# Kernel optimization log

Measured on AMD Instinct MI355X. Metric: run time of the kernel, lower is better.

Reference implementation:

```python
import jax, jax.numpy as jnp
import numpy as np

D = 1024
H = 16
HD = D // H
B = 2
S = 2048


def setup_inputs() -> dict:
    key = jax.random.key(0)
    ks = jax.random.split(key, 9)
    sc = 1.0 / np.sqrt(D)
    return {
        "x": jax.random.normal(ks[0], (B, S, D), dtype=jnp.float32),
        "attention_mask": jnp.ones((B, S), dtype=jnp.int32),
        "Wq": jax.random.normal(ks[1], (D, D), dtype=jnp.float32) * sc,
        "bq": jax.random.normal(ks[2], (D,), dtype=jnp.float32) * 0.02,
        "Wk": jax.random.normal(ks[3], (D, D), dtype=jnp.float32) * sc,
        "bk": jax.random.normal(ks[4], (D,), dtype=jnp.float32) * 0.02,
        "Wv": jax.random.normal(ks[5], (D, D), dtype=jnp.float32) * sc,
        "bv": jax.random.normal(ks[6], (D,), dtype=jnp.float32) * 0.02,
        "Wo": jax.random.normal(ks[7], (D, D), dtype=jnp.float32) * sc,
        "bo": jax.random.normal(ks[8], (D,), dtype=jnp.float32) * 0.02,
    }


def reference(x, attention_mask, Wq, bq, Wk, bk, Wv, bv, Wo, bo):
    Bb, Ss, d = x.shape
    # projections (torch Linear: x @ W.T + b; here W stored as [in,out])
    q = (x @ Wq + bq).reshape(Bb, Ss, H, HD).transpose(0, 2, 1, 3)  # [B,H,S,hd]
    k = (x @ Wk + bk).reshape(Bb, Ss, H, HD).transpose(0, 2, 1, 3)
    v = (x @ Wv + bv).reshape(Bb, Ss, H, HD).transpose(0, 2, 1, 3)
    dots = jnp.einsum("bhqd,bhkd->bhqk", q, k) / np.sqrt(HD)  # [B,H,S,S]
    causal = jnp.triu(jnp.ones((Ss, Ss), dtype=bool), k=1)  # True above diagonal
    dots = jnp.where(causal[None, None], -jnp.inf, dots)
    pad = (attention_mask == 0)[:, None, None, :]  # [B,1,1,S]
    dots = jnp.where(pad, -jnp.inf, dots)
    scores = jax.nn.softmax(dots, axis=-1)
    o = jnp.einsum("bhqk,bhkd->bhqd", scores, v)  # [B,H,S,hd]
    o = o.transpose(0, 2, 1, 3).reshape(Bb, Ss, d)
    return o @ Wo + bo
```

## Files before the change

kernel.cpp:

```cpp
#include <hip/hip_runtime.h>

#define D_  1024
#define H_  16
#define HD_ 64
#define B_  2
#define S_  2048
#define M_  (B_*S_)

typedef _Float16 f16;
typedef _Float16 f16x8 __attribute__((ext_vector_type(8)));
typedef _Float16 f16x4 __attribute__((ext_vector_type(4)));
typedef _Float16 f16x2 __attribute__((ext_vector_type(2)));
typedef __fp16   h16x2 __attribute__((ext_vector_type(2)));
typedef float    f32x4 __attribute__((ext_vector_type(4)));

#define GLOAD_LDS16(g, l) \
  __builtin_amdgcn_global_load_lds((__attribute__((address_space(1))) const void*)(g), \
                                   (__attribute__((address_space(3))) void*)(l), 16, 0, 0)

__global__ void k_cvt_x(const float* __restrict__ x, f16* __restrict__ xb) {
  int i = blockIdx.x * blockDim.x + threadIdx.x;
  float4 v = ((const float4*)x)[i];
  f16x4 o = { (f16)v.x, (f16)v.y, (f16)v.z, (f16)v.w };
  ((f16x4*)xb)[i] = o;
}

__global__ void k_twt4(const float* __restrict__ Wq, const float* __restrict__ Wk,
                       const float* __restrict__ Wv, const float* __restrict__ Wo,
                       f16* __restrict__ WT) {
  __shared__ float t[32][33];
  int z = blockIdx.z;
  const float* W = (z == 0) ? Wq : (z == 1) ? Wk : (z == 2) ? Wv : Wo;
  f16* out = WT + (size_t)z * D_ * D_;
  int n0 = blockIdx.x * 32, k0 = blockIdx.y * 32;
  int tx = threadIdx.x, ty = threadIdx.y;
  #pragma unroll
  for (int i = 0; i < 4; i++)
    t[ty + i*8][tx] = W[(size_t)(k0 + ty + i*8) * D_ + n0 + tx];
  __syncthreads();
  #pragma unroll
  for (int i = 0; i < 4; i++)
    out[(size_t)(n0 + ty + i*8) * D_ + k0 + tx] = (f16)t[tx][ty + i*8];
}

template<int MODE>
__device__ __forceinline__ void gemm_body(const f16* __restrict__ A,
                                          const f16* __restrict__ Bt,
                                          const float* __restrict__ bias,
                                          void* __restrict__ Cout) {
  __shared__ __align__(16) f16 lA[2][128 * 32];
  __shared__ __align__(16) f16 lB[2][128 * 32];
  const int tid = threadIdx.x;
  const int wv = tid >> 6, lane = tid & 63;
  const int m0 = blockIdx.y * 128, n0 = blockIdx.x * 128;
  const int fr = lane & 15, fg = lane >> 4;
  const int wm = wv >> 1, wn = wv & 1;
  const int srow = (lane >> 2), skk = (lane & 3) * 8;
  f32x4 acc[4][4] = {};

#define G_STAGE(k0_, c_) do { \
    _Pragma("unroll") \
    for (int it_ = 0; it_ < 2; ++it_) { \
      int ch_ = wv + it_ * 4; \
      int row_ = ch_ * 16 + srow; \
      GLOAD_LDS16(A  + (size_t)(m0 + row_) * D_ + (k0_) + skk, &lA[c_][ch_ * 512]); \
      GLOAD_LDS16(Bt + (size_t)(n0 + row_) * D_ + (k0_) + skk, &lB[c_][ch_ * 512]); \
    } \
  } while (0)

  G_STAGE(0, 0);
  __syncthreads();

  int c = 0;
  for (int k0 = 0; k0 < D_; k0 += 32) {
    if (k0 + 32 < D_) G_STAGE(k0 + 32, c ^ 1);
    f16x8 a[4], b[4];
    #pragma unroll
    for (int i = 0; i < 4; i++) a[i] = *(const f16x8*)&lA[c][(wm*64 + i*16 + fr) * 32 + fg * 8];
    #pragma unroll
    for (int j = 0; j < 4; j++) b[j] = *(const f16x8*)&lB[c][(wn*64 + j*16 + fr) * 32 + fg * 8];
    #pragma unroll
    for (int i = 0; i < 4; i++)
      #pragma unroll
      for (int j = 0; j < 4; j++)
        acc[i][j] = __builtin_amdgcn_mfma_f32_16x16x32_f16(a[i], b[j], acc[i][j], 0, 0, 0);
    __syncthreads();
    c ^= 1;
  }
#undef G_STAGE

  #pragma unroll
  for (int i = 0; i < 4; i++) {
    #pragma unroll
    for (int j = 0; j < 4; j++) {
      int grow0 = m0 + wm*64 + i*16 + fg*4;
      int gcol  = n0 + wn*64 + j*16 + fr;
      float bb = bias[gcol & (D_ - 1)];
      #pragma unroll
      for (int r = 0; r < 4; r++) {
        float val = acc[i][j][r] + bb;
        int grow = grow0 + r;
        if (MODE == 0) {
          int z = gcol >> 10, gl = gcol & (D_ - 1);
          int b = grow >> 11, s = grow & (S_ - 1);
          int h = gl >> 6,  hd = gl & (HD_ - 1);
          ((f16*)Cout)[(size_t)z * (M_ * D_) +
                       ((size_t)(b * H_ + h) * S_ + s) * HD_ + hd] = (f16)val;
        } else {
          ((float*)Cout)[(size_t)grow * D_ + gcol] = val;
        }
      }
    }
  }
}

__global__ __launch_bounds__(256) void k_gemm_qkv(const f16* __restrict__ A,
                                                  const f16* __restrict__ WT0,
                                                  const float* __restrict__ bq,
                                                  const float* __restrict__ bk,
                                                  const float* __restrict__ bv,
                                                  f16* __restrict__ qkv) {
  const int n0 = blockIdx.x * 128;
  const float* bias = (n0 < 1024) ? bq : (n0 < 2048) ? bk : bv;
  gemm_body<0>(A, WT0, bias, qkv);
}

__global__ __launch_bounds__(256) void k_gemm_out(const f16* __restrict__ A,
                                                  const f16* __restrict__ Bt,
                                                  const float* __restrict__ bias,
                                                  float* __restrict__ Cout) {
  gemm_body<1>(A, Bt, bias, Cout);
}

#define POFF 8.65617025f

__global__ __launch_bounds__(256) void k_attn(const f16* __restrict__ Qh,
                                              const f16* __restrict__ Kh,
                                              const f16* __restrict__ Vh,
                                              const int* __restrict__ am,
                                              f16* __restrict__ OpA, f16* __restrict__ OpB,
                                              float* __restrict__ lpA, float* __restrict__ lpB) {
  __shared__ __align__(16) f16 kt[2][64 * 64];
  __shared__ __align__(16) f16 vt[2][64 * 64];
  __shared__ __align__(16) f16 pl[4][32 * 64];

  const int tid = threadIdx.x;
  const int wv = tid >> 6, lane = tid & 63;
  const int fr = lane & 15, fg = lane >> 4;

  const int d = blockIdx.x;
  const int bh = d & 31;
  const int m  = (d >> 5) & 7;
  const int typeB = d >> 8;
  const int b = bh >> 4, h = bh & 15;
  (void)h;

  f16*   Op = typeB ? OpB : OpA;
  float* lp = typeB ? lpB : lpA;

  const f16* Qb = Qh + (size_t)bh * S_ * HD_;
  const f16* Kb = Kh + (size_t)bh * S_ * HD_;
  const f16* Vb = Vh + (size_t)bh * S_ * HD_;
  const int* amb = am + b * S_;
  f16* plw = pl[wv];

  volatile int* flag = (volatile int*)&pl[0][0];
  if (tid == 0) *flag = 1;
  __syncthreads();
  {
    int mv = 1;
    #pragma unroll
    for (int i = 0; i < 8; ++i) mv &= amb[tid * 8 + i];
    if (!mv) *flag = 0;
  }
  __syncthreads();
  const bool allv = (*flag != 0);

  const f16 qs = (f16)0.18033688f;
  const int ksrc = 8 * ((lane & 7) ^ (lane >> 3));
  const int swz = (fr & 7) << 3;
  const int vkk = (tid >> 3) * 2, vd0 = (tid & 7) * 8;
  const int vswz2 = (tid & 3) << 4;
  const f32x4 cinit = { -POFF, -POFF, -POFF, -POFF };
  const f16 one_ = (f16)1.0f;
  const f16x8 onesf = { one_, one_, one_, one_, one_, one_, one_, one_ };

#define STAGE_K(t_, c_) do { \
    const f16* kp_ = Kb + (size_t)((t_) * 64) * HD_; \
    GLOAD_LDS16(kp_ + (size_t)((wv*2+0)*8 + (lane >> 3)) * HD_ + ksrc, &kt[c_][(wv*2+0)*512]); \
    GLOAD_LDS16(kp_ + (size_t)((wv*2+1)*8 + (lane >> 3)) * HD_ + ksrc, &kt[c_][(wv*2+1)*512]); \
  } while (0)

#define LOAD_V(t_) do { \
    const f16* vp_ = Vb + (size_t)((t_) * 64 + vkk) * HD_ + vd0; \
    vA = *(const f16x8*)vp_; vBr = *(const f16x8*)(vp_ + HD_); \
  } while (0)

#define WRITE_V(c_) do { \
    _Pragma("unroll") \
    for (int j_ = 0; j_ < 8; ++j_) { \
      f16x2 pr_ = { vA[j_], vBr[j_] }; \
      *(f16x2*)&vt[c_][(vd0 + j_) * 64 + ((vkk ^ (j_ << 3)) ^ vswz2)] = pr_; \
    } \
  } while (0)

  f16x8 vA, vBr;

  auto run_half = [&](int qt, int t0, int t1) {
    const int q0w = qt * 128 + wv * 32;

    f16x8 qf[2][2];
    #pragma unroll
    for (int rt = 0; rt < 2; ++rt) {
      f16x8 r0 = *(const f16x8*)&Qb[(size_t)(q0w + rt*16 + fr) * HD_ + fg*8];
      f16x8 r1 = *(const f16x8*)&Qb[(size_t)(q0w + rt*16 + fr) * HD_ + 32 + fg*8];
      qf[rt][0] = r0 * qs; qf[rt][1] = r1 * qs;
    }

    f32x4 accO[2][4] = {};
    f32x4 accL[2] = {};

    STAGE_K(t0, 0);
    LOAD_V(t0);
    WRITE_V(0);
    __syncthreads();

    int c = 0;
    for (int t = t0; t < t1; ++t) {
      const int kb = t * 64;
      const bool pre = (t + 1 < t1);
      if (pre) { STAGE_K(t + 1, c ^ 1); LOAD_V(t + 1); }

      const int dq = q0w - kb;
      if (dq + 31 >= 0) {
        int tm1 = (dq + 31) >> 4; if (tm1 > 3) tm1 = 3;
        int tm0 = (dq + 15) >> 4; if (tm0 > 3) tm0 = 3;
        const bool fullb = (dq >= 63);

        f32x4 s[2][4];
        #pragma unroll
        for (int rt = 0; rt < 2; ++rt)
          #pragma unroll
          for (int tt = 0; tt < 4; ++tt) s[rt][tt] = cinit;

        __builtin_amdgcn_s_setprio(1);
        #pragma unroll
        for (int tt = 0; tt < 4; ++tt) {
          if (tt <= tm1) {
            const int kr = (tt*16 + fr) * 64;
            f16x8 kf0 = *(const f16x8*)&kt[c][kr + ((     fg*8) ^ swz)];
            f16x8 kf1 = *(const f16x8*)&kt[c][kr + ((32 + fg*8) ^ swz)];
            s[1][tt] = __builtin_amdgcn_mfma_f32_16x16x32_f16(kf0, qf[1][0], s[1][tt], 0, 0, 0);
            s[1][tt] = __builtin_amdgcn_mfma_f32_16x16x32_f16(kf1, qf[1][1], s[1][tt], 0, 0, 0);
            if (tt <= tm0) {
              s[0][tt] = __builtin_amdgcn_mfma_f32_16x16x32_f16(kf0, qf[0][0], s[0][tt], 0, 0, 0);
              s[0][tt] = __builtin_amdgcn_mfma_f32_16x16x32_f16(kf1, qf[0][1], s[0][tt], 0, 0, 0);
            }
          }
        }
        __builtin_amdgcn_s_setprio(0);

        #pragma unroll
        for (int rt = 0; rt < 2; ++rt) {
          const int tmr = rt ? tm1 : tm0;
          if (tmr < 0) continue;
          const int thr = dq + rt*16 + fr;
          #pragma unroll
          for (int tt = 0; tt < 4; ++tt) {
            union { f16x4 v; h16x2 h[2]; } pk;
            pk.v = (f16x4){};
            if (tt <= tmr) {
              float p[4];
              if (allv) {
                #pragma unroll
                for (int r = 0; r < 4; ++r) {
                  float sv = s[rt][tt][r];
                  if (!fullb) sv = (tt*16 + fg*4 + r <= thr) ? sv : -1e30f;
                  p[r] = exp2f(sv);
                }
              } else {
                int4 a4 = *(const int4*)&amb[kb + tt*16 + fg*4];
                #pragma unroll
                for (int r = 0; r < 4; ++r) {
                  float sv = s[rt][tt][r];
                  if (!fullb) sv = (tt*16 + fg*4 + r <= thr) ? sv : -1e30f;
                  float pv = exp2f(sv);
                  int mr_ = (r == 0) ? a4.x : (r == 1) ? a4.y : (r == 2) ? a4.z : a4.w;
                  p[r] = mr_ ? pv : 0.0f;
                }
              }
              pk.h[0] = __builtin_amdgcn_cvt_pkrtz(p[0], p[1]);
              pk.h[1] = __builtin_amdgcn_cvt_pkrtz(p[2], p[3]);
            }
            *(f16x4*)&plw[(rt*16 + fr) * 64 + ((tt*16 + fg*4) ^ swz)] = pk.v;
          }
        }

        __builtin_amdgcn_s_setprio(1);
        #pragma unroll
        for (int ks = 0; ks < 2; ++ks) {
          if (ks <= (tm1 >> 1)) {
            f16x8 vf[4];
            #pragma unroll
            for (int nt = 0; nt < 4; ++nt)
              vf[nt] = *(const f16x8*)&vt[c][(nt*16 + fr) * 64 +
                           ((ks*32 + fg*8) ^ swz ^ (((2*nt + (fr >> 3)) & 3) << 4))];
            #pragma unroll
            for (int rt = 0; rt < 2; ++rt) {
              const int tmr = rt ? tm1 : tm0;
              if (tmr >= 0 && ks <= (tmr >> 1)) {
                f16x8 pa = *(const f16x8*)&plw[(rt*16 + fr) * 64 + ((ks*32 + fg*8) ^ swz)];
                #pragma unroll
                for (int nt = 0; nt < 4; ++nt)
                  accO[rt][nt] = __builtin_amdgcn_mfma_f32_16x16x32_f16(pa, vf[nt], accO[rt][nt], 0, 0, 0);
                accL[rt] = __builtin_amdgcn_mfma_f32_16x16x32_f16(pa, onesf, accL[rt], 0, 0, 0);
              }
            }
          }
        }
        __builtin_amdgcn_s_setprio(0);
      }

      if (pre) WRITE_V(c ^ 1);
      __syncthreads();
      c ^= 1;
    }

    #pragma unroll
    for (int rt = 0; rt < 2; ++rt) {
      if (fr == 0) {
        #pragma unroll
        for (int r = 0; r < 4; ++r)
          lp[(size_t)bh * S_ + q0w + rt*16 + fg*4 + r] = accL[rt][r];
      }
      f16* Oprow = Op + (size_t)bh * (S_ * HD_);
      #pragma unroll
      for (int nt = 0; nt < 4; ++nt) {
        int col = nt*16 + fr;
        #pragma unroll
        for (int r = 0; r < 4; ++r) {
          int row = q0w + rt*16 + fg*4 + r;
          Oprow[(size_t)row * HD_ + col] = (f16)accO[rt][nt][r];
        }
      }
    }
  };

  const int qtA = m, qtB = 15 - m;
  if (!typeB) {
    run_half(qtA, 0, qtA + 1);
    run_half(qtB, 0, qtB + 1);
  } else {
    run_half(qtA, qtA + 1, 2 * (qtA + 1));
    run_half(qtB, qtB + 1, 2 * (qtB + 1));
  }

#undef STAGE_K
#undef LOAD_V
#undef WRITE_V
}

__global__ __launch_bounds__(256) void k_comb(const f16* __restrict__ OA,
                                              const f16* __restrict__ OB,
                                              const float* __restrict__ lA,
                                              const float* __restrict__ lB,
                                              f16* __restrict__ Obf) {
  int gid = blockIdx.x * 256 + threadIdx.x;
  int seg = gid & 7, rowg = gid >> 3;
  int bh = rowg >> 11, row = rowg & 2047;
  f16x8 a  = ((const f16x8*)OA)[gid];
  f16x8 b2 = ((const f16x8*)OB)[gid];
  float inv = __builtin_amdgcn_rcpf(lA[rowg] + lB[rowg]);
  f16x8 o;
  #pragma unroll
  for (int j = 0; j < 8; ++j) o[j] = (f16)(((float)a[j] + (float)b2[j]) * inv);
  int bb = bh >> 4, hh = bh & 15;
  *(f16x8*)&Obf[((size_t)(bb * S_ + row)) * D_ + hh * 64 + seg * 8] = o;
}

extern "C" void kernel_launch(void* const* d_in, const int* in_sizes, int n_in,
                              void* d_out, int out_size, void* d_ws, size_t ws_size,
                              hipStream_t stream) {
  const float* x  = (const float*)d_in[0];
  const int*   am = (const int*)d_in[1];
  const float* Wq = (const float*)d_in[2];
  const float* bq = (const float*)d_in[3];
  const float* Wk = (const float*)d_in[4];
  const float* bk = (const float*)d_in[5];
  const float* Wv = (const float*)d_in[6];
  const float* bv = (const float*)d_in[7];
  const float* Wo = (const float*)d_in[8];
  const float* bo = (const float*)d_in[9];

  char* ws = (char*)d_ws;
  f16*   xb  = (f16*)(ws);
  f16*   wt  = (f16*)(ws + (8u  << 20));
  f16*   qkv = (f16*)(ws + (16u << 20));
  f16*   OpA = (f16*)(ws + (40u << 20));
  f16*   OpB = xb;
  float* lpA = (float*)(ws + (8u << 20));
  float* lpB = (float*)(ws + (8u << 20) + (256u << 10));
  f16*   Obf = qkv;

  k_cvt_x<<<4096, 256, 0, stream>>>(x, xb);

  dim3 tb(32, 8), tg4(32, 32, 4);
  k_twt4<<<tg4, tb, 0, stream>>>(Wq, Wk, Wv, Wo, wt);

  k_gemm_qkv<<<dim3(24, 32), 256, 0, stream>>>(xb, wt, bq, bk, bv, qkv);

  k_attn<<<dim3(512), 256, 0, stream>>>(qkv,
                                        qkv + (size_t)M_ * D_,
                                        qkv + 2 * (size_t)M_ * D_,
                                        am, OpA, OpB, lpA, lpB);

  k_comb<<<dim3(2048), 256, 0, stream>>>(OpA, OpB, lpA, lpB, Obf);

  k_gemm_out<<<dim3(8, 32), 256, 0, stream>>>(Obf, wt + 3 * (size_t)(D_ * D_), bo,
                                              (float*)d_out);
}
```

Before: 124.6 us.

## Split causal attention KV range three ways across 768 blocks

```diff
diff --git a/kernel.cpp b/kernel.cpp
--- a/kernel.cpp
+++ b/kernel.cpp
@@ -138,8 +138,10 @@
                                               const f16* __restrict__ Kh,
                                               const f16* __restrict__ Vh,
                                               const int* __restrict__ am,
-                                              f16* __restrict__ OpA, f16* __restrict__ OpB,
-                                              float* __restrict__ lpA, float* __restrict__ lpB) {
+                                              f16* __restrict__ Op0, f16* __restrict__ Op1,
+                                              f16* __restrict__ Op2,
+                                              float* __restrict__ lp0, float* __restrict__ lp1,
+                                              float* __restrict__ lp2) {
   __shared__ __align__(16) f16 kt[2][64 * 64];
   __shared__ __align__(16) f16 vt[2][64 * 64];
   __shared__ __align__(16) f16 pl[4][32 * 64];
@@ -148,15 +150,14 @@
   const int wv = tid >> 6, lane = tid & 63;
   const int fr = lane & 15, fg = lane >> 4;
 
-  const int d = blockIdx.x;
-  const int bh = d & 31;
-  const int m  = (d >> 5) & 7;
-  const int typeB = d >> 8;
-  const int b = bh >> 4, h = bh & 15;
-  (void)h;
-
-  f16*   Op = typeB ? OpB : OpA;
-  float* lp = typeB ? lpB : lpA;
+  const int dd = blockIdx.x;
+  const int bh = dd & 31;
+  const int m  = (dd >> 5) & 7;
+  const int sp = dd >> 8;
+  const int b = bh >> 4;
+
+  f16*   Op = (sp == 0) ? Op0 : (sp == 1) ? Op1 : Op2;
+  float* lp = (sp == 0) ? lp0 : (sp == 1) ? lp1 : lp2;
 
   const f16* Qb = Qh + (size_t)bh * S_ * HD_;
   const f16* Kb = Kh + (size_t)bh * S_ * HD_;
@@ -208,122 +209,123 @@
 
   auto run_half = [&](int qt, int t0, int t1) {
     const int q0w = qt * 128 + wv * 32;
-
-    f16x8 qf[2][2];
-    #pragma unroll
-    for (int rt = 0; rt < 2; ++rt) {
-      f16x8 r0 = *(const f16x8*)&Qb[(size_t)(q0w + rt*16 + fr) * HD_ + fg*8];
-      f16x8 r1 = *(const f16x8*)&Qb[(size_t)(q0w + rt*16 + fr) * HD_ + 32 + fg*8];
-      qf[rt][0] = r0 * qs; qf[rt][1] = r1 * qs;
-    }
-
     f32x4 accO[2][4] = {};
     f32x4 accL[2] = {};
 
-    STAGE_K(t0, 0);
-    LOAD_V(t0);
-    WRITE_V(0);
-    __syncthreads();
-
-    int c = 0;
-    for (int t = t0; t < t1; ++t) {
-      const int kb = t * 64;
-      const bool pre = (t + 1 < t1);
-      if (pre) { STAGE_K(t + 1, c ^ 1); LOAD_V(t + 1); }
-
-      const int dq = q0w - kb;
-      if (dq + 31 >= 0) {
-        int tm1 = (dq + 31) >> 4; if (tm1 > 3) tm1 = 3;
-        int tm0 = (dq + 15) >> 4; if (tm0 > 3) tm0 = 3;
-        const bool fullb = (dq >= 63);
-
-        f32x4 s[2][4];
-        #pragma unroll
-        for (int rt = 0; rt < 2; ++rt)
+    if (t0 < t1) {
+      f16x8 qf[2][2];
+      #pragma unroll
+      for (int rt = 0; rt < 2; ++rt) {
+        f16x8 r0 = *(const f16x8*)&Qb[(size_t)(q0w + rt*16 + fr) * HD_ + fg*8];
+        f16x8 r1 = *(const f16x8*)&Qb[(size_t)(q0w + rt*16 + fr) * HD_ + 32 + fg*8];
+        qf[rt][0] = r0 * qs; qf[rt][1] = r1 * qs;
+      }
+
+      STAGE_K(t0, 0);
+      LOAD_V(t0);
+      WRITE_V(0);
+      __syncthreads();
+
+      int c = 0;
+      for (int t = t0; t < t1; ++t) {
+        const int kb = t * 64;
+        const bool pre = (t + 1 < t1);
+        if (pre) { STAGE_K(t + 1, c ^ 1); LOAD_V(t + 1); }
+
+        const int dq = q0w - kb;
+        if (dq + 31 >= 0) {
+          int tm1 = (dq + 31) >> 4; if (tm1 > 3) tm1 = 3;
+          int tm0 = (dq + 15) >> 4; if (tm0 > 3) tm0 = 3;
+          const bool fullb = (dq >= 63);
+
+          f32x4 s[2][4];
           #pragma unroll
-          for (int tt = 0; tt < 4; ++tt) s[rt][tt] = cinit;
-
-        __builtin_amdgcn_s_setprio(1);
-        #pragma unroll
-        for (int tt = 0; tt < 4; ++tt) {
-          if (tt <= tm1) {
-            const int kr = (tt*16 + fr) * 64;
-            f16x8 kf0 = *(const f16x8*)&kt[c][kr + ((     fg*8) ^ swz)];
-            f16x8 kf1 = *(const f16x8*)&kt[c][kr + ((32 + fg*8) ^ swz)];
-            s[1][tt] = __builtin_amdgcn_mfma_f32_16x16x32_f16(kf0, qf[1][0], s[1][tt], 0, 0, 0);
-            s[1][tt] = __builtin_amdgcn_mfma_f32_16x16x32_f16(kf1, qf[1][1], s[1][tt], 0, 0, 0);
-            if (tt <= tm0) {
-              s[0][tt] = __builtin_amdgcn_mfma_f32_16x16x32_f16(kf0, qf[0][0], s[0][tt], 0, 0, 0);
-              s[0][tt] = __builtin_amdgcn_mfma_f32_16x16x32_f16(kf1, qf[0][1], s[0][tt], 0, 0, 0);
-            }
-          }
-        }
-        __builtin_amdgcn_s_setprio(0);
-
-        #pragma unroll
-        for (int rt = 0; rt < 2; ++rt) {
-          const int tmr = rt ? tm1 : tm0;
-          if (tmr < 0) continue;
-          const int thr = dq + rt*16 + fr;
+          for (int rt = 0; rt < 2; ++rt)
+            #pragma unroll
+            for (int tt = 0; tt < 4; ++tt) s[rt][tt] = cinit;
+
+          __builtin_amdgcn_s_setprio(1);
           #pragma unroll
           for (int tt = 0; tt < 4; ++tt) {
-            union { f16x4 v; h16x2 h[2]; } pk;
-            pk.v = (f16x4){};
-            if (tt <= tmr) {
-              float p[4];
-              if (allv) {
-                #pragma unroll
-                for (int r = 0; r < 4; ++r) {
-                  float sv = s[rt][tt][r];
-                  if (!fullb) sv = (tt*16 + fg*4 + r <= thr) ? sv : -1e30f;
-                  p[r] = exp2f(sv);
-                }
-              } else {
-                int4 a4 = *(const int4*)&amb[kb + tt*16 + fg*4];
-                #pragma unroll
-                for (int r = 0; r < 4; ++r) {
-                  float sv = s[rt][tt][r];
-                  if (!fullb) sv = (tt*16 + fg*4 + r <= thr) ? sv : -1e30f;
-                  float pv = exp2f(sv);
-                  int mr_ = (r == 0) ? a4.x : (r == 1) ? a4.y : (r == 2) ? a4.z : a4.w;
-                  p[r] = mr_ ? pv : 0.0f;
-                }
-              }
-              pk.h[0] = __builtin_amdgcn_cvt_pkrtz(p[0], p[1]);
-              pk.h[1] = __builtin_amdgcn_cvt_pkrtz(p[2], p[3]);
-            }
-            *(f16x4*)&plw[(rt*16 + fr) * 64 + ((tt*16 + fg*4) ^ swz)] = pk.v;
-          }
-        }
-
-        __builtin_amdgcn_s_setprio(1);
-        #pragma unroll
-        for (int ks = 0; ks < 2; ++ks) {
-          if (ks <= (tm1 >> 1)) {
-            f16x8 vf[4];
-            #pragma unroll
-            for (int nt = 0; nt < 4; ++nt)
-              vf[nt] = *(const f16x8*)&vt[c][(nt*16 + fr) * 64 +
-                           ((ks*32 + fg*8) ^ swz ^ (((2*nt + (fr >> 3)) & 3) << 4))];
-            #pragma unroll
-            for (int rt = 0; rt < 2; ++rt) {
-              const int tmr = rt ? tm1 : tm0;
-              if (tmr >= 0 && ks <= (tmr >> 1)) {
-                f16x8 pa = *(const f16x8*)&plw[(rt*16 + fr) * 64 + ((ks*32 + fg*8) ^ swz)];
-                #pragma unroll
-                for (int nt = 0; nt < 4; ++nt)
-                  accO[rt][nt] = __builtin_amdgcn_mfma_f32_16x16x32_f16(pa, vf[nt], accO[rt][nt], 0, 0, 0);
-                accL[rt] = __builtin_amdgcn_mfma_f32_16x16x32_f16(pa, onesf, accL[rt], 0, 0, 0);
+            if (tt <= tm1) {
+              const int kr = (tt*16 + fr) * 64;
+              f16x8 kf0 = *(const f16x8*)&kt[c][kr + ((     fg*8) ^ swz)];
+              f16x8 kf1 = *(const f16x8*)&kt[c][kr + ((32 + fg*8) ^ swz)];
+              s[1][tt] = __builtin_amdgcn_mfma_f32_16x16x32_f16(kf0, qf[1][0], s[1][tt], 0, 0, 0);
+              s[1][tt] = __builtin_amdgcn_mfma_f32_16x16x32_f16(kf1, qf[1][1], s[1][tt], 0, 0, 0);
+              if (tt <= tm0) {
+                s[0][tt] = __builtin_amdgcn_mfma_f32_16x16x32_f16(kf0, qf[0][0], s[0][tt], 0, 0, 0);
+                s[0][tt] = __builtin_amdgcn_mfma_f32_16x16x32_f16(kf1, qf[0][1], s[0][tt], 0, 0, 0);
               }
             }
           }
+          __builtin_amdgcn_s_setprio(0);
+
+          #pragma unroll
+          for (int rt = 0; rt < 2; ++rt) {
+            const int tmr = rt ? tm1 : tm0;
+            if (tmr < 0) continue;
+            const int thr = dq + rt*16 + fr;
+            #pragma unroll
+            for (int tt = 0; tt < 4; ++tt) {
+              union { f16x4 v; h16x2 h[2]; } pk;
+              pk.v = (f16x4){};
+              if (tt <= tmr) {
+                float p[4];
+                if (allv) {
+                  #pragma unroll
+                  for (int r = 0; r < 4; ++r) {
+                    float sv = s[rt][tt][r];
+                    if (!fullb) sv = (tt*16 + fg*4 + r <= thr) ? sv : -1e30f;
+                    p[r] = exp2f(sv);
+                  }
+                } else {
+                  int4 a4 = *(const int4*)&amb[kb + tt*16 + fg*4];
+                  #pragma unroll
+                  for (int r = 0; r < 4; ++r) {
+                    float sv = s[rt][tt][r];
+                    if (!fullb) sv = (tt*16 + fg*4 + r <= thr) ? sv : -1e30f;
+                    float pv = exp2f(sv);
+                    int mr_ = (r == 0) ? a4.x : (r == 1) ? a4.y : (r == 2) ? a4.z : a4.w;
+                    p[r] = mr_ ? pv : 0.0f;
+                  }
+                }
+                pk.h[0] = __builtin_amdgcn_cvt_pkrtz(p[0], p[1]);
+                pk.h[1] = __builtin_amdgcn_cvt_pkrtz(p[2], p[3]);
+              }
+              *(f16x4*)&plw[(rt*16 + fr) * 64 + ((tt*16 + fg*4) ^ swz)] = pk.v;
+            }
+          }
+
+          __builtin_amdgcn_s_setprio(1);
+          #pragma unroll
+          for (int ks = 0; ks < 2; ++ks) {
+            if (ks <= (tm1 >> 1)) {
+              f16x8 vf[4];
+              #pragma unroll
+              for (int nt = 0; nt < 4; ++nt)
+                vf[nt] = *(const f16x8*)&vt[c][(nt*16 + fr) * 64 +
+                             ((ks*32 + fg*8) ^ swz ^ (((2*nt + (fr >> 3)) & 3) << 4))];
+              #pragma unroll
+              for (int rt = 0; rt < 2; ++rt) {
+                const int tmr = rt ? tm1 : tm0;
+                if (tmr >= 0 && ks <= (tmr >> 1)) {
+                  f16x8 pa = *(const f16x8*)&plw[(rt*16 + fr) * 64 + ((ks*32 + fg*8) ^ swz)];
+                  #pragma unroll
+                  for (int nt = 0; nt < 4; ++nt)
+                    accO[rt][nt] = __builtin_amdgcn_mfma_f32_16x16x32_f16(pa, vf[nt], accO[rt][nt], 0, 0, 0);
+                  accL[rt] = __builtin_amdgcn_mfma_f32_16x16x32_f16(pa, onesf, accL[rt], 0, 0, 0);
+                }
+              }
+            }
+          }
+          __builtin_amdgcn_s_setprio(0);
         }
-        __builtin_amdgcn_s_setprio(0);
+
+        if (pre) WRITE_V(c ^ 1);
+        __syncthreads();
+        c ^= 1;
       }
-
-      if (pre) WRITE_V(c ^ 1);
-      __syncthreads();
-      c ^= 1;
     }
 
     #pragma unroll
@@ -346,34 +348,33 @@
     }
   };
 
-  const int qtA = m, qtB = 15 - m;
-  if (!typeB) {
-    run_half(qtA, 0, qtA + 1);
-    run_half(qtB, 0, qtB + 1);
-  } else {
-    run_half(qtA, qtA + 1, 2 * (qtA + 1));
-    run_half(qtB, qtB + 1, 2 * (qtB + 1));
-  }
+  const int nA = 2 * (m + 1), nB = 2 * (16 - m), rs = 2 - sp;
+  run_half(m,      (nA * sp) / 3, (nA * (sp + 1)) / 3);
+  run_half(15 - m, (nB * rs) / 3, (nB * (rs + 1)) / 3);
 
 #undef STAGE_K
 #undef LOAD_V
 #undef WRITE_V
 }
 
-__global__ __launch_bounds__(256) void k_comb(const f16* __restrict__ OA,
-                                              const f16* __restrict__ OB,
-                                              const float* __restrict__ lA,
-                                              const float* __restrict__ lB,
-                                              f16* __restrict__ Obf) {
+__global__ __launch_bounds__(256) void k_comb3(const f16* __restrict__ O0,
+                                               const f16* __restrict__ O1,
+                                               const f16* __restrict__ O2,
+                                               const float* __restrict__ l0,
+                                               const float* __restrict__ l1,
+                                               const float* __restrict__ l2,
+                                               f16* __restrict__ Obf) {
   int gid = blockIdx.x * 256 + threadIdx.x;
   int seg = gid & 7, rowg = gid >> 3;
   int bh = rowg >> 11, row = rowg & 2047;
-  f16x8 a  = ((const f16x8*)OA)[gid];
-  f16x8 b2 = ((const f16x8*)OB)[gid];
-  float inv = __builtin_amdgcn_rcpf(lA[rowg] + lB[rowg]);
+  f16x8 a  = ((const f16x8*)O0)[gid];
+  f16x8 b2 = ((const f16x8*)O1)[gid];
+  f16x8 c3 = ((const f16x8*)O2)[gid];
+  float inv = __builtin_amdgcn_rcpf(l0[rowg] + l1[rowg] + l2[rowg]);
   f16x8 o;
   #pragma unroll
-  for (int j = 0; j < 8; ++j) o[j] = (f16)(((float)a[j] + (float)b2[j]) * inv);
+  for (int j = 0; j < 8; ++j)
+    o[j] = (f16)((((float)a[j] + (float)b2[j]) + (float)c3[j]) * inv);
   int bb = bh >> 4, hh = bh & 15;
   *(f16x8*)&Obf[((size_t)(bb * S_ + row)) * D_ + hh * 64 + seg * 8] = o;
 }
@@ -396,10 +397,12 @@
   f16*   xb  = (f16*)(ws);
   f16*   wt  = (f16*)(ws + (8u  << 20));
   f16*   qkv = (f16*)(ws + (16u << 20));
-  f16*   OpA = (f16*)(ws + (40u << 20));
-  f16*   OpB = xb;
-  float* lpA = (float*)(ws + (8u << 20));
-  float* lpB = (float*)(ws + (8u << 20) + (256u << 10));
+  f16*   Op0 = (f16*)(ws + (40u << 20));
+  f16*   Op1 = xb;
+  f16*   Op2 = (f16*)d_out;
+  float* lp0 = (float*)(ws + (8u << 20));
+  float* lp1 = (float*)(ws + (8u << 20) + (256u << 10));
+  float* lp2 = (float*)(ws + (8u << 20) + (512u << 10));
   f16*   Obf = qkv;
 
   k_cvt_x<<<4096, 256, 0, stream>>>(x, xb);
@@ -409,12 +412,12 @@
 
   k_gemm_qkv<<<dim3(24, 32), 256, 0, stream>>>(xb, wt, bq, bk, bv, qkv);
 
-  k_attn<<<dim3(512), 256, 0, stream>>>(qkv,
+  k_attn<<<dim3(768), 256, 0, stream>>>(qkv,
                                         qkv + (size_t)M_ * D_,
                                         qkv + 2 * (size_t)M_ * D_,
-                                        am, OpA, OpB, lpA, lpB);
-
-  k_comb<<<dim3(2048), 256, 0, stream>>>(OpA, OpB, lpA, lpB, Obf);
+                                        am, Op0, Op1, Op2, lp0, lp1, lp2);
+
+  k_comb3<<<dim3(2048), 256, 0, stream>>>(Op0, Op1, Op2, lp0, lp1, lp2, Obf);
 
   k_gemm_out<<<dim3(8, 32), 256, 0, stream>>>(Obf, wt + 3 * (size_t)(D_ * D_), bo,
                                               (float*)d_out);
```

Result: slower. 141.1 us (+13.3%).
